# Kernel tuning notes

Measured on AMD Instinct MI355X. Metric: run time of the kernel, lower is better.

The kernel has to match this reference:

```python
import jax, jax.numpy as jnp
import numpy as np

B, N, T, F_IN = 32, 512, 12, 128
K, CF, TF, PRED = 3, 64, 64, 12


def _cheb_polys(n, k):
    # identity adjacency -> scaled Laplacian = -I; T0=I, T1=-I, Tk = 2(-I)T_{k-1} - T_{k-2}
    L = -np.eye(n, dtype=np.float32)
    polys = [np.eye(n, dtype=np.float32)]
    if k > 1:
        polys.append(L.copy())
    for i in range(2, k):
        polys.append(2 * L @ polys[i - 1] - polys[i - 2])
    return jnp.asarray(np.stack(polys))  # (K, N, N)


def _conv2d(x, w, b, stride, pad):
    # x: (B,C,H,W), w: (O,I,kh,kw) torch layout
    y = jax.lax.conv_general_dilated(x, w, window_strides=stride, padding=pad,
                                     dimension_numbers=("NCHW", "OIHW", "NCHW"))
    return y + b[None, :, None, None]


def _block(x, cheb, theta, tw, tb, rw, rb, lg, lb, stride):
    # x: (B,N,Fin,T); cheb: (K,N,N); theta: (K,Fin,Fout)
    # fused Chebyshev conv over all t and k: out[b,m,o,t] = sum_{k,n,f} x[b,n,f,t] cheb[k,n,m] theta[k,f,o]
    s = jax.nn.relu(jnp.einsum("bnft,knm,kfo->bmot", x, cheb, theta))  # (B,N,CF,T)
    t = _conv2d(jnp.transpose(s, (0, 2, 1, 3)), tw, tb, (1, stride), ((0, 0), (1, 1)))  # (B,TF,N,T')
    r = _conv2d(jnp.transpose(x, (0, 2, 1, 3)), rw, rb, (1, stride), ((0, 0), (0, 0)))  # (B,TF,N,T')
    h = jnp.transpose(jax.nn.relu(r + t), (0, 3, 2, 1))  # (B,T',N,TF)
    mu = h.mean(-1, keepdims=True)
    var = ((h - mu) ** 2).mean(-1, keepdims=True)
    h = (h - mu) * jax.lax.rsqrt(var + 1e-5) * lg + lb
    return jnp.transpose(h, (0, 2, 3, 1))  # (B,N,TF,T')


def setup_inputs() -> dict:
    key = jax.random.key(0)
    ks = jax.random.split(key, 8)
    rn = lambda k, shape, s=0.05: jax.random.normal(k, shape, dtype=jnp.float32) * s
    return {
        "x": jax.random.normal(ks[0], (B, N, T, F_IN), dtype=jnp.float32),
        "theta0": rn(ks[1], (K, F_IN, CF)),
        "tconv_w0": rn(ks[2], (TF, CF, 1, 3)),
        "tconv_b0": jnp.zeros((TF,), jnp.float32),
        "rconv_w0": rn(ks[3], (TF, F_IN, 1, 1)),
        "rconv_b0": jnp.zeros((TF,), jnp.float32),
        "ln_g0": jnp.ones((TF,), jnp.float32),
        "ln_b0": jnp.zeros((TF,), jnp.float32),
        "theta1": rn(ks[4], (K, TF, CF)),
        "tconv_w1": rn(ks[5], (TF, CF, 1, 3)),
        "tconv_b1": jnp.zeros((TF,), jnp.float32),
        "rconv_w1": rn(ks[6], (TF, TF, 1, 1)),
        "rconv_b1": jnp.zeros((TF,), jnp.float32),
        "ln_g1": jnp.ones((TF,), jnp.float32),
        "ln_b1": jnp.zeros((TF,), jnp.float32),
        "fconv_w": rn(ks[7], (PRED, T, 1, TF)),
        "fconv_b": jnp.zeros((PRED,), jnp.float32),
    }


def reference(x, theta0, tconv_w0, tconv_b0, rconv_w0, rconv_b0, ln_g0, ln_b0,
              theta1, tconv_w1, tconv_b1, rconv_w1, rconv_b1, ln_g1, ln_b1,
              fconv_w, fconv_b):
    cheb = _cheb_polys(x.shape[1], theta0.shape[0])
    h = jnp.transpose(x, (0, 1, 3, 2))  # (B,N,F_in,T)
    h = _block(h, cheb, theta0, tconv_w0, tconv_b0, rconv_w0, rconv_b0, ln_g0, ln_b0, 1)
    h = _block(h, cheb, theta1, tconv_w1, tconv_b1, rconv_w1, rconv_b1, ln_g1, ln_b1, 1)
    hf = jnp.transpose(h, (0, 3, 1, 2))  # (B,T',N,TF)
    out = _conv2d(hf, fconv_w, fconv_b, (1, 1), ((0, 0), (0, 0)))[:, :, :, -1]  # (B,PRED,N)
    return jnp.transpose(out, (0, 2, 1))  # (B,N,PRED)
```

## Files before the change

kernel.cpp:

```cpp
#include <hip/hip_runtime.h>


typedef __attribute__((ext_vector_type(8))) short bf16x8;
typedef __attribute__((ext_vector_type(4))) float f32x4;

#define FR_W1   0
#define FR_TW0  32
#define FR_W2   56
#define FR_TW1  72
#define FR_FW   96
#define N_FRAGS 120

__device__ __forceinline__ unsigned short f2bf(float f) {
    unsigned u = __builtin_bit_cast(unsigned, f);
    return (unsigned short)((u + 0x7FFFu + ((u >> 16) & 1u)) >> 16);
}

__global__ void prep(const float* __restrict__ th0, const float* __restrict__ tw0,
                     const float* __restrict__ rw0, const float* __restrict__ th1,
                     const float* __restrict__ tw1, const float* __restrict__ rw1,
                     const float* __restrict__ fw,  short* __restrict__ wsb)
{
    int e = blockIdx.x * 256 + threadIdx.x;
    if (e >= N_FRAGS * 512) return;
    int frag = e >> 9;
    int l    = (e >> 3) & 63;
    int i    = e & 7;
    int kif  = ((l >> 4) << 3) + i;
    int nif  = l & 15;
    float val = 0.f;
    if (frag < 32) {
        int ks = frag >> 3, nt = frag & 7;
        int k = ks * 32 + kif, n = nt * 16 + nif;
        if (n < 64) val = th0[k*64+n] - th0[8192 + k*64+n] + th0[16384 + k*64+n];
        else        val = rw0[(n - 64) * 128 + k];
    } else if (frag < 56) {
        int q = frag - 32; int dt = q >> 3, ks = (q >> 2) & 1, nt = q & 3;
        int c = ks * 32 + kif, o = nt * 16 + nif;
        val = tw0[o * 192 + c * 3 + dt];
    } else if (frag < 72) {
        int q = frag - 56; int ks = q >> 3, nt = q & 7;
        int k = ks * 32 + kif, n = nt * 16 + nif;
        if (n < 64) val = th1[k*64+n] - th1[4096 + k*64+n] + th1[8192 + k*64+n];
        else        val = rw1[(n - 64) * 64 + k];
    } else if (frag < 96) {
        int q = frag - 72; int dt = q >> 3, ks = (q >> 2) & 1, nt = q & 3;
        int c = ks * 32 + kif, o = nt * 16 + nif;
        val = tw1[o * 192 + c * 3 + dt];
    } else {
        int ks = frag - 96; int k = ks * 32 + kif; int po = nif;
        val = (po < 12) ? fw[po * 768 + k] : 0.f;
    }
    wsb[e] = (short)f2bf(val);
}

#define LDS_SY(w)  (LDS + (w) * 6144)
#define LDS_FB     (LDS + 24576)
#define LDS_PB     ((float*)(LDS + 49152))

__global__ __launch_bounds__(256, 2) void mstgcn_mfma(
    const float* __restrict__ x,   const short* __restrict__ wsb,
    const float* __restrict__ tb0, const float* __restrict__ rb0,
    const float* __restrict__ lg0, const float* __restrict__ lb0,
    const float* __restrict__ tb1, const float* __restrict__ rb1,
    const float* __restrict__ lg1, const float* __restrict__ lb1,
    const float* __restrict__ fb,  float* __restrict__ out)
{
    __shared__ __align__(16) char LDS[53248];

    const int lane = threadIdx.x & 63;
    const int wave = threadIdx.x >> 6;
    const int l15  = lane & 15;
    const int l4   = lane >> 4;
    const int pair0 = blockIdx.x * 16 + wave * 4;

    char* syB = LDS_SY(wave);

    auto ldfrag = [&](int f) -> bf16x8 {
        return *(const bf16x8*)(wsb + f * 512 + lane * 8);
    };

    int rowA[3], tA[3];
    long gbase[3];
    #pragma unroll
    for (int mt = 0; mt < 3; ++mt) {
        int r = mt * 16 + l15;
        int p = r / 12;
        rowA[mt] = r;
        tA[mt]   = r - p * 12;
        gbase[mt] = ((long)(pair0 + p) * 12 + tA[mt]) * 128;
    }

    f32x4 accS[3][4] = {}, accR[3][4] = {};
    #pragma unroll
    for (int ks = 0; ks < 4; ++ks) {
        bf16x8 a[3];
        #pragma unroll
        for (int mt = 0; mt < 3; ++mt) {
            const float* p = x + gbase[mt] + ks * 32 + l4 * 8;
            float v[8];
            *(float4*)(v)     = *(const float4*)(p);
            *(float4*)(v + 4) = *(const float4*)(p + 4);
            bf16x8 af;
            #pragma unroll
            for (int j = 0; j < 8; ++j) af[j] = (short)f2bf(v[j]);
            a[mt] = af;
        }
        #pragma unroll
        for (int nt = 0; nt < 4; ++nt) {
            bf16x8 b = ldfrag(FR_W1 + ks * 8 + nt);
            #pragma unroll
            for (int mt = 0; mt < 3; ++mt)
                accS[mt][nt] = __builtin_amdgcn_mfma_f32_16x16x32_bf16(a[mt], b, accS[mt][nt], 0, 0, 0);
        }
        #pragma unroll
        for (int nt = 0; nt < 4; ++nt) {
            bf16x8 b = ldfrag(FR_W1 + ks * 8 + 4 + nt);
            #pragma unroll
            for (int mt = 0; mt < 3; ++mt)
                accR[mt][nt] = __builtin_amdgcn_mfma_f32_16x16x32_bf16(a[mt], b, accR[mt][nt], 0, 0, 0);
        }
    }
    #pragma unroll
    for (int mt = 0; mt < 3; ++mt)
        #pragma unroll
        for (int j = 0; j < 4; ++j) {
            int row = mt * 16 + l4 * 4 + j;
            int sw  = (row & 7) << 4;
            #pragma unroll
            for (int nt = 0; nt < 4; ++nt) {
                int col = nt * 16 + l15;
                *(short*)(syB + row * 128 + ((col * 2) ^ sw)) =
                    (short)f2bf(fmaxf(accS[mt][nt][j], 0.f));
            }
        }

    #pragma unroll
    for (int dt = 0; dt < 3; ++dt) {
        #pragma unroll
        for (int ks = 0; ks < 2; ++ks) {
            bf16x8 a[3];
            #pragma unroll
            for (int mt = 0; mt < 3; ++mt) {
                int ts    = tA[mt] + dt - 1;
                bool ok   = (ts >= 0) && (ts < 12);
                int srow  = ok ? (rowA[mt] + dt - 1) : rowA[mt];
                int kb    = (ks * 32 + l4 * 8) * 2;
                bf16x8 av = *(const bf16x8*)(syB + srow * 128 + (kb ^ ((srow & 7) << 4)));
                a[mt] = ok ? av : (bf16x8)(short)0;
            }
            #pragma unroll
            for (int nt = 0; nt < 4; ++nt) {
                bf16x8 b = ldfrag(FR_TW0 + dt * 8 + ks * 4 + nt);
                #pragma unroll
                for (int mt = 0; mt < 3; ++mt)
                    accR[mt][nt] = __builtin_amdgcn_mfma_f32_16x16x32_bf16(a[mt], b, accR[mt][nt], 0, 0, 0);
            }
        }
    }

    {
        float bv[4], lgv[4], lbv[4];
        #pragma unroll
        for (int nt = 0; nt < 4; ++nt) {
            int col = nt * 16 + l15;
            bv[nt]  = rb0[col] + tb0[col];
            lgv[nt] = lg0[col];
            lbv[nt] = lb0[col];
        }
        #pragma unroll
        for (int mt = 0; mt < 3; ++mt)
            #pragma unroll
            for (int j = 0; j < 4; ++j) {
                float v[4], sm = 0.f, sq = 0.f;
                #pragma unroll
                for (int nt = 0; nt < 4; ++nt) {
                    v[nt] = fmaxf(accR[mt][nt][j] + bv[nt], 0.f);
                    sm += v[nt]; sq += v[nt] * v[nt];
                }
                #pragma unroll
                for (int m = 8; m; m >>= 1) {
                    sm += __shfl_xor(sm, m, 64);
                    sq += __shfl_xor(sq, m, 64);
                }
                float mu = sm * 0.015625f;
                float is = rsqrtf(sq * 0.015625f - mu * mu + 1e-5f);
                int row = mt * 16 + l4 * 4 + j;
                int sw  = (row & 7) << 4;
                #pragma unroll
                for (int nt = 0; nt < 4; ++nt) {
                    int col = nt * 16 + l15;
                    *(short*)(syB + row * 128 + ((col * 2) ^ sw)) =
                        (short)f2bf((v[nt] - mu) * is * lgv[nt] + lbv[nt]);
                }
            }
    }

    #pragma unroll
    for (int mt = 0; mt < 3; ++mt)
        #pragma unroll
        for (int nt = 0; nt < 4; ++nt) { accS[mt][nt] = (f32x4)0.f; accR[mt][nt] = (f32x4)0.f; }
    #pragma unroll
    for (int ks = 0; ks < 2; ++ks) {
        bf16x8 a[3];
        #pragma unroll
        for (int mt = 0; mt < 3; ++mt) {
            int row = rowA[mt];
            int kb  = (ks * 32 + l4 * 8) * 2;
            a[mt] = *(const bf16x8*)(syB + row * 128 + (kb ^ ((row & 7) << 4)));
        }
        #pragma unroll
        for (int nt = 0; nt < 4; ++nt) {
            bf16x8 b = ldfrag(FR_W2 + ks * 8 + nt);
            #pragma unroll
            for (int mt = 0; mt < 3; ++mt)
                accS[mt][nt] = __builtin_amdgcn_mfma_f32_16x16x32_bf16(a[mt], b, accS[mt][nt], 0, 0, 0);
        }
        #pragma unroll
        for (int nt = 0; nt < 4; ++nt) {
            bf16x8 b = ldfrag(FR_W2 + ks * 8 + 4 + nt);
            #pragma unroll
            for (int mt = 0; mt < 3; ++mt)
                accR[mt][nt] = __builtin_amdgcn_mfma_f32_16x16x32_bf16(a[mt], b, accR[mt][nt], 0, 0, 0);
        }
    }
    #pragma unroll
    for (int mt = 0; mt < 3; ++mt)
        #pragma unroll
        for (int j = 0; j < 4; ++j) {
            int row = mt * 16 + l4 * 4 + j;
            int sw  = (row & 7) << 4;
            #pragma unroll
            for (int nt = 0; nt < 4; ++nt) {
                int col = nt * 16 + l15;
                *(short*)(syB + row * 128 + ((col * 2) ^ sw)) =
                    (short)f2bf(fmaxf(accS[mt][nt][j], 0.f));
            }
        }

    #pragma unroll
    for (int dt = 0; dt < 3; ++dt) {
        #pragma unroll
        for (int ks = 0; ks < 2; ++ks) {
            bf16x8 a[3];
            #pragma unroll
            for (int mt = 0; mt < 3; ++mt) {
                int ts    = tA[mt] + dt - 1;
                bool ok   = (ts >= 0) && (ts < 12);
                int srow  = ok ? (rowA[mt] + dt - 1) : rowA[mt];
                int kb    = (ks * 32 + l4 * 8) * 2;
                bf16x8 av = *(const bf16x8*)(syB + srow * 128 + (kb ^ ((srow & 7) << 4)));
                a[mt] = ok ? av : (bf16x8)(short)0;
            }
            #pragma unroll
            for (int nt = 0; nt < 4; ++nt) {
                bf16x8 b = ldfrag(FR_TW1 + dt * 8 + ks * 4 + nt);
                #pragma unroll
                for (int mt = 0; mt < 3; ++mt)
                    accR[mt][nt] = __builtin_amdgcn_mfma_f32_16x16x32_bf16(a[mt], b, accR[mt][nt], 0, 0, 0);
            }
        }
    }

    {
        float bv[4], lgv[4], lbv[4];
        #pragma unroll
        for (int nt = 0; nt < 4; ++nt) {
            int col = nt * 16 + l15;
            bv[nt]  = rb1[col] + tb1[col];
            lgv[nt] = lg1[col];
            lbv[nt] = lb1[col];
        }
        #pragma unroll
        for (int mt = 0; mt < 3; ++mt)
            #pragma unroll
            for (int j = 0; j < 4; ++j) {
                float v[4], sm = 0.f, sq = 0.f;
                #pragma unroll
                for (int nt = 0; nt < 4; ++nt) {
                    v[nt] = fmaxf(accR[mt][nt][j] + bv[nt], 0.f);
                    sm += v[nt]; sq += v[nt] * v[nt];
                }
                #pragma unroll
                for (int m = 8; m; m >>= 1) {
                    sm += __shfl_xor(sm, m, 64);
                    sq += __shfl_xor(sq, m, 64);
                }
                float mu = sm * 0.015625f;
                float is = rsqrtf(sq * 0.015625f - mu * mu + 1e-5f);
                int row = mt * 16 + l4 * 4 + j;
                int p   = row / 12;
                int t   = row - p * 12;
                int gp  = wave * 4 + p;
                int sw  = (gp & 7) << 4;
                #pragma unroll
                for (int nt = 0; nt < 4; ++nt) {
                    int k = t * 64 + nt * 16 + l15;
                    *(short*)(LDS_FB + gp * 1536 + ((k * 2) ^ sw)) =
                        (short)f2bf((v[nt] - mu) * is * lgv[nt] + lbv[nt]);
                }
            }
    }
    __syncthreads();

    {
        f32x4 accF = (f32x4)0.f;
        #pragma unroll
        for (int q = 0; q < 6; ++q) {
            int ks = wave * 6 + q;
            int kb = (ks * 32 + l4 * 8) * 2;
            bf16x8 a = *(const bf16x8*)(LDS_FB + l15 * 1536 + (kb ^ ((l15 & 7) << 4)));
            bf16x8 b = ldfrag(FR_FW + ks);
            accF = __builtin_amdgcn_mfma_f32_16x16x32_bf16(a, b, accF, 0, 0, 0);
        }
        #pragma unroll
        for (int j = 0; j < 4; ++j)
            LDS_PB[wave * 256 + (l4 * 4 + j) * 16 + l15] = accF[j];
    }
    __syncthreads();
    {
        int tid = threadIdx.x;
        int gp = tid >> 4, po = tid & 15;
        if (po < 12) {
            float s = LDS_PB[gp * 16 + po] + LDS_PB[256 + gp * 16 + po]
                    + LDS_PB[512 + gp * 16 + po] + LDS_PB[768 + gp * 16 + po];
            out[(long)(blockIdx.x * 16 + gp) * 12 + po] = s + fb[po];
        }
    }
}

extern "C" void kernel_launch(void* const* d_in, const int* in_sizes, int n_in,
                              void* d_out, int out_size, void* d_ws, size_t ws_size,
                              hipStream_t stream)
{
    (void)in_sizes; (void)n_in; (void)out_size; (void)ws_size;
    const float* x   = (const float*)d_in[0];
    const float* th0 = (const float*)d_in[1];
    const float* tw0 = (const float*)d_in[2];
    const float* tb0 = (const float*)d_in[3];
    const float* rw0 = (const float*)d_in[4];
    const float* rb0 = (const float*)d_in[5];
    const float* lg0 = (const float*)d_in[6];
    const float* lb0 = (const float*)d_in[7];
    const float* th1 = (const float*)d_in[8];
    const float* tw1 = (const float*)d_in[9];
    const float* tb1 = (const float*)d_in[10];
    const float* rw1 = (const float*)d_in[11];
    const float* rb1 = (const float*)d_in[12];
    const float* lg1 = (const float*)d_in[13];
    const float* lb1 = (const float*)d_in[14];
    const float* fw  = (const float*)d_in[15];
    const float* fb  = (const float*)d_in[16];
    float* out = (float*)d_out;
    short* wsb = (short*)d_ws;

    prep<<<240, 256, 0, stream>>>(th0, tw0, rw0, th1, tw1, rw1, fw, wsb);
    mstgcn_mfma<<<1024, 256, 0, stream>>>(x, wsb, tb0, rb0, lg0, lb0,
                                          tb1, rb1, lg1, lb1, fb, out);
}
```

Baseline: 60.79 us.

## Keep final conv per-wave in private LDS, drop block syncs, raise occupancy

The final prediction convolution now reads each wave's own normalized block-1 output from its private LDS slice, so the shared feature buffer, the partial-sum buffer and both __syncthreads are removed. Each wave runs all 24 K-steps itself with two accumulators and writes its 4 pairs directly. Block LDS shrinks from 52 KB to 24 KB and launch bounds rise to 4 blocks per CU to improve occupancy. The manual bf16 rounding is also replaced by the HIP intrinsic conversion. The risks are more MFMA work per wave, with only 4 of 16 rows useful, and register pressure under the tighter launch bound.

```diff
diff --git a/kernel.cpp b/kernel.cpp
--- a/kernel.cpp
+++ b/kernel.cpp
@@ -1,4 +1,5 @@
 #include <hip/hip_runtime.h>
+#include <hip/hip_bf16.h>
 
 
 typedef __attribute__((ext_vector_type(8))) short bf16x8;
@@ -14,6 +15,12 @@
 __device__ __forceinline__ unsigned short f2bf(float f) {
     unsigned u = __builtin_bit_cast(unsigned, f);
     return (unsigned short)((u + 0x7FFFu + ((u >> 16) & 1u)) >> 16);
+}
+
+__device__ __forceinline__ unsigned short hcvt(float f) {
+    union { __hip_bfloat16 h; unsigned short u; } cv;
+    cv.h = __float2bfloat16(f);
+    return cv.u;
 }
 
 __global__ void prep(const float* __restrict__ th0, const float* __restrict__ tw0,
@@ -55,10 +62,8 @@
 }
 
 #define LDS_SY(w)  (LDS + (w) * 6144)
-#define LDS_FB     (LDS + 24576)
-#define LDS_PB     ((float*)(LDS + 49152))
-
-__global__ __launch_bounds__(256, 2) void mstgcn_mfma(
+
+__global__ __launch_bounds__(256, 4) void mstgcn_mfma(
     const float* __restrict__ x,   const short* __restrict__ wsb,
     const float* __restrict__ tb0, const float* __restrict__ rb0,
     const float* __restrict__ lg0, const float* __restrict__ lb0,
@@ -66,7 +71,7 @@
     const float* __restrict__ lg1, const float* __restrict__ lb1,
     const float* __restrict__ fb,  float* __restrict__ out)
 {
-    __shared__ __align__(16) char LDS[53248];
+    __shared__ __align__(16) char LDS[24576];
 
     const int lane = threadIdx.x & 63;
     const int wave = threadIdx.x >> 6;
@@ -103,7 +108,7 @@
             *(float4*)(v + 4) = *(const float4*)(p + 4);
             bf16x8 af;
             #pragma unroll
-            for (int j = 0; j < 8; ++j) af[j] = (short)f2bf(v[j]);
+            for (int j = 0; j < 8; ++j) af[j] = (short)hcvt(v[j]);
             a[mt] = af;
         }
         #pragma unroll
@@ -131,7 +136,7 @@
             for (int nt = 0; nt < 4; ++nt) {
                 int col = nt * 16 + l15;
                 *(short*)(syB + row * 128 + ((col * 2) ^ sw)) =
-                    (short)f2bf(fmaxf(accS[mt][nt][j], 0.f));
+                    (short)hcvt(fmaxf(accS[mt][nt][j], 0.f));
             }
         }
 
@@ -191,7 +196,7 @@
                 for (int nt = 0; nt < 4; ++nt) {
                     int col = nt * 16 + l15;
                     *(short*)(syB + row * 128 + ((col * 2) ^ sw)) =
-                        (short)f2bf((v[nt] - mu) * is * lgv[nt] + lbv[nt]);
+                        (short)hcvt((v[nt] - mu) * is * lgv[nt] + lbv[nt]);
                 }
             }
     }
@@ -234,7 +239,7 @@
             for (int nt = 0; nt < 4; ++nt) {
                 int col = nt * 16 + l15;
                 *(short*)(syB + row * 128 + ((col * 2) ^ sw)) =
-                    (short)f2bf(fmaxf(accS[mt][nt][j], 0.f));
+                    (short)hcvt(fmaxf(accS[mt][nt][j], 0.f));
             }
         }
 
@@ -289,42 +294,39 @@
                 float mu = sm * 0.015625f;
                 float is = rsqrtf(sq * 0.015625f - mu * mu + 1e-5f);
                 int row = mt * 16 + l4 * 4 + j;
-                int p   = row / 12;
-                int t   = row - p * 12;
-                int gp  = wave * 4 + p;
-                int sw  = (gp & 7) << 4;
+                int sw  = (row & 7) << 4;
                 #pragma unroll
                 for (int nt = 0; nt < 4; ++nt) {
-                    int k = t * 64 + nt * 16 + l15;
-                    *(short*)(LDS_FB + gp * 1536 + ((k * 2) ^ sw)) =
-                        (short)f2bf((v[nt] - mu) * is * lgv[nt] + lbv[nt]);
-                }
-            }
-    }
-    __syncthreads();
+                    int col = nt * 16 + l15;
+                    *(short*)(syB + row * 128 + ((col * 2) ^ sw)) =
+                        (short)hcvt((v[nt] - mu) * is * lgv[nt] + lbv[nt]);
+                }
+            }
+    }
 
     {
-        f32x4 accF = (f32x4)0.f;
-        #pragma unroll
-        for (int q = 0; q < 6; ++q) {
-            int ks = wave * 6 + q;
-            int kb = (ks * 32 + l4 * 8) * 2;
-            bf16x8 a = *(const bf16x8*)(LDS_FB + l15 * 1536 + (kb ^ ((l15 & 7) << 4)));
-            bf16x8 b = ldfrag(FR_FW + ks);
-            accF = __builtin_amdgcn_mfma_f32_16x16x32_bf16(a, b, accF, 0, 0, 0);
-        }
-        #pragma unroll
-        for (int j = 0; j < 4; ++j)
-            LDS_PB[wave * 256 + (l4 * 4 + j) * 16 + l15] = accF[j];
-    }
-    __syncthreads();
-    {
-        int tid = threadIdx.x;
-        int gp = tid >> 4, po = tid & 15;
-        if (po < 12) {
-            float s = LDS_PB[gp * 16 + po] + LDS_PB[256 + gp * 16 + po]
-                    + LDS_PB[512 + gp * 16 + po] + LDS_PB[768 + gp * 16 + po];
-            out[(long)(blockIdx.x * 16 + gp) * 12 + po] = s + fb[po];
+        f32x4 acc0 = (f32x4)0.f, acc1 = (f32x4)0.f;
+        int p   = (l15 < 4) ? l15 : 0;
+        #pragma unroll
+        for (int ks = 0; ks < 24; ks += 2) {
+            {
+                int t = ks >> 1, f0 = l4 * 8;
+                int row = p * 12 + t;
+                bf16x8 a = *(const bf16x8*)(syB + row * 128 + ((f0 * 2) ^ ((row & 7) << 4)));
+                acc0 = __builtin_amdgcn_mfma_f32_16x16x32_bf16(a, ldfrag(FR_FW + ks), acc0, 0, 0, 0);
+            }
+            {
+                int t = ks >> 1, f0 = 32 + l4 * 8;
+                int row = p * 12 + t;
+                bf16x8 a = *(const bf16x8*)(syB + row * 128 + ((f0 * 2) ^ ((row & 7) << 4)));
+                acc1 = __builtin_amdgcn_mfma_f32_16x16x32_bf16(a, ldfrag(FR_FW + ks + 1), acc1, 0, 0, 0);
+            }
+        }
+        if (l4 == 0 && l15 < 12) {
+            float fbv = fb[l15];
+            #pragma unroll
+            for (int j = 0; j < 4; ++j)
+                out[(long)(pair0 + j) * 12 + l15] = acc0[j] + acc1[j] + fbv;
         }
     }
 }
```

Result: slower. 110.7 us (+82.1%).
